# Kernel optimization log

Measured on AMD Instinct MI355X. Metric: run time of the kernel, lower is better.

Reference implementation:

```python
import jax, jax.numpy as jnp
import numpy as np

N_HEADS = 16


def setup_inputs() -> dict:
    key = jax.random.key(0)
    k1, k2, k3 = jax.random.split(key, 3)
    n_embed = 1024
    b, t = 4, 2048
    x = jax.random.normal(k1, (b, t, n_embed), dtype=jnp.float32)
    # Linear weights stored as [in, out]; y = x @ W + b (same math as torch Linear).
    Wqkv = jax.random.normal(k2, (n_embed, 3 * n_embed), dtype=jnp.float32) * (n_embed ** -0.5)
    bqkv = jnp.zeros((3 * n_embed,), dtype=jnp.float32)
    Wout = jax.random.normal(k3, (n_embed, n_embed), dtype=jnp.float32) * (n_embed ** -0.5)
    bout = jnp.zeros((n_embed,), dtype=jnp.float32)
    return {"x": x, "Wqkv": Wqkv, "bqkv": bqkv, "Wout": Wout, "bout": bout}


def reference(x, Wqkv, bqkv, Wout, bout):
    b, t, n_embed = x.shape
    hs = n_embed // N_HEADS
    qkv = x @ Wqkv + bqkv  # [b, t, 3*n_embed]
    q, k, v = jnp.split(qkv, 3, axis=-1)
    # b t (h hs) -> b h t hs
    def to_heads(u):
        return u.reshape(b, t, N_HEADS, hs).transpose(0, 2, 1, 3)
    q, k, v = to_heads(q), to_heads(k), to_heads(v)
    scale = 1.0 / jnp.sqrt(jnp.asarray(hs, dtype=x.dtype))
    scores = jnp.einsum('bhqd,bhkd->bhqk', q, k) * scale  # [b, h, t, t]
    causal = jnp.tril(jnp.ones((t, t), dtype=bool))
    scores = jnp.where(causal, scores, jnp.finfo(scores.dtype).min)
    attn = jax.nn.softmax(scores, axis=-1)
    out = jnp.einsum('bhqk,bhkd->bhqd', attn, v)  # [b, h, t, hs]
    out = out.transpose(0, 2, 1, 3).reshape(b, t, n_embed)  # b h t hs -> b t (h hs)
    return out @ Wout + bout
```

## Files before the change

kernel.cpp:

```cpp
#include <hip/hip_runtime.h>
#include <hip/hip_bf16.h>
#include <stdint.h>

typedef unsigned short u16;
typedef __bf16 bf16x8 __attribute__((ext_vector_type(8)));
typedef float f32x4 __attribute__((ext_vector_type(4)));
typedef u16 ushort8 __attribute__((ext_vector_type(8)));
typedef short short4v __attribute__((ext_vector_type(4)));

__device__ __forceinline__ u16 f2bf(float f) {
    unsigned int u = __builtin_bit_cast(unsigned int, f);
    u += 0x7fffu + ((u >> 16) & 1u);
    return (u16)(u >> 16);
}

#define MFMA16(a, b, c) __builtin_amdgcn_mfma_f32_16x16x32_bf16( \
    __builtin_bit_cast(bf16x8, a), __builtin_bit_cast(bf16x8, b), c, 0, 0, 0)

#if defined(__has_builtin)
#if __has_builtin(__builtin_amdgcn_exp2f)
#define EXP2(x) __builtin_amdgcn_exp2f(x)
#endif
#endif
#ifndef EXP2
#define EXP2(x) __expf((x) * 0.69314718f)
#endif

__device__ __forceinline__ void async16(void* lds, const void* g) {
    __builtin_amdgcn_global_load_lds(
        (const __attribute__((address_space(1))) unsigned int*)(uintptr_t)g,
        (__attribute__((address_space(3))) unsigned int*)(unsigned int)(uintptr_t)lds,
        16, 0, 0);
}

__global__ __launch_bounds__(256) void convert_bf16(
    const float* __restrict__ src, u16* __restrict__ dst)
{
    int i = blockIdx.x * 256 + threadIdx.x;
    float4 f0 = ((const float4*)src)[i * 2];
    float4 f1 = ((const float4*)src)[i * 2 + 1];
    ushort8 v;
    v[0]=f2bf(f0.x); v[1]=f2bf(f0.y); v[2]=f2bf(f0.z); v[3]=f2bf(f0.w);
    v[4]=f2bf(f1.x); v[5]=f2bf(f1.y); v[6]=f2bf(f1.z); v[7]=f2bf(f1.w);
    ((ushort8*)dst)[i] = v;
}

__global__ __launch_bounds__(256) void transpose_convert(
    const float* __restrict__ src, u16* __restrict__ dst, int N, int K)
{
    __shared__ u16 T[64][68];
    const int k0 = blockIdx.x * 64, n0 = blockIdx.y * 64;
    const int tid = threadIdx.x;
    const int rr = tid >> 4, cc = (tid & 15) * 4;
    #pragma unroll
    for (int rnd = 0; rnd < 4; ++rnd) {
        int r = rr + rnd * 16;
        float4 f = *(const float4*)&src[(size_t)(k0 + r) * N + n0 + cc];
        u16 v[4] = {f2bf(f.x), f2bf(f.y), f2bf(f.z), f2bf(f.w)};
        *(unsigned long long*)&T[r][cc] = *(unsigned long long*)v;
    }
    __syncthreads();
    #pragma unroll
    for (int rnd = 0; rnd < 4; ++rnd) {
        int rn = rr + rnd * 16;
        u16 v[4];
        #pragma unroll
        for (int j = 0; j < 4; ++j) v[j] = T[cc + j][rn];
        *(unsigned long long*)&dst[(size_t)(n0 + rn) * K + k0 + cc] =
            *(unsigned long long*)v;
    }
}

__device__ __forceinline__ void gemm_mainloop(
    const u16* __restrict__ A, const u16* __restrict__ Bt,
    u16* As, u16* Bs, int m0, int n0, int tid, f32x4 acc[4][4])
{
    const int lane = tid & 63, w = tid >> 6;
    const int lr = lane & 15, quad = lane >> 4;
    const int wm = w & 1, wn = w >> 1;
    const int grow = lane & 7, gchunk = lane >> 3;

    for (int k0 = 0; k0 < 1024; k0 += 64) {
        __syncthreads();
        #pragma unroll
        for (int r = 0; r < 4; ++r) {
            int rb = w * 4 + r;
            async16(As + rb * 512,
                    A + (size_t)(m0 + rb * 8 + grow) * 1024 + k0 + gchunk * 8);
            async16(Bs + rb * 512,
                    Bt + (size_t)(n0 + rb * 8 + grow) * 1024 + k0 + gchunk * 8);
        }
        __syncthreads();
        #pragma unroll
        for (int kk = 0; kk < 2; ++kk) {
            ushort8 a[4], b[4];
            #pragma unroll
            for (int mt = 0; mt < 4; ++mt) {
                int rb = wm * 8 + mt * 2 + (lr >> 3);
                a[mt] = *(ushort8*)&As[rb * 512 + (kk * 4 + quad) * 64 + (lr & 7) * 8];
            }
            #pragma unroll
            for (int nt = 0; nt < 4; ++nt) {
                int rb = wn * 8 + nt * 2 + (lr >> 3);
                b[nt] = *(ushort8*)&Bs[rb * 512 + (kk * 4 + quad) * 64 + (lr & 7) * 8];
            }
            #pragma unroll
            for (int mt = 0; mt < 4; ++mt)
                #pragma unroll
                for (int nt = 0; nt < 4; ++nt)
                    acc[mt][nt] = MFMA16(a[mt], b[nt], acc[mt][nt]);
        }
    }
}

__global__ __launch_bounds__(256) void qkv_gemm(
    const u16* __restrict__ xb, const u16* __restrict__ Wt,
    const float* __restrict__ bias, u16* __restrict__ qkvb)
{
    __shared__ u16 As[8192], Bs[8192];
    const int m0 = blockIdx.x * 128, n0 = blockIdx.y * 128;
    const int tid = threadIdx.x;
    f32x4 acc[4][4] = {};
    gemm_mainloop(xb, Wt, As, Bs, m0, n0, tid, acc);

    const int lane = tid & 63, w = tid >> 6;
    const int lr = lane & 15, quad = lane >> 4;
    const int wm = w & 1, wn = w >> 1;
    const int which = n0 >> 10;
    float bv[4];
    #pragma unroll
    for (int nt = 0; nt < 4; ++nt) bv[nt] = bias[n0 + wn * 64 + nt * 16 + lr];

    if (which == 2) {
        u16* vT = qkvb + (size_t)2 * 8388608;
        #pragma unroll
        for (int nt = 0; nt < 4; ++nt) {
            int n = n0 + wn * 64 + nt * 16 + lr;
            int hh = (n >> 6) & 15, d = n & 63;
            #pragma unroll
            for (int mt = 0; mt < 4; ++mt) {
                int mbase = m0 + wm * 64 + mt * 16 + quad * 4;
                int b_idx = mbase >> 11, t0 = mbase & 2047;
                short4v o4;
                #pragma unroll
                for (int reg = 0; reg < 4; ++reg)
                    o4[reg] = (short)f2bf(acc[mt][nt][reg] + bv[nt]);
                *(short4v*)&vT[((size_t)(b_idx * 16 + hh) * 64 + d) * 2048 + t0] = o4;
            }
        }
    } else {
        u16* dst = qkvb + (size_t)which * 8388608;
        #pragma unroll
        for (int mt = 0; mt < 4; ++mt)
          #pragma unroll
          for (int nt = 0; nt < 4; ++nt) {
            int n = n0 + wn * 64 + nt * 16 + lr;
            int hh = (n >> 6) & 15, d = n & 63;
            #pragma unroll
            for (int reg = 0; reg < 4; ++reg) {
                int m = m0 + wm * 64 + mt * 16 + quad * 4 + reg;
                int b_idx = m >> 11, t_idx = m & 2047;
                dst[(((size_t)(b_idx * 16 + hh) * 2048 + t_idx) << 6) + d] =
                    f2bf(acc[mt][nt][reg] + bv[nt]);
            }
          }
    }
}

__global__ __launch_bounds__(256) void out_gemm(
    const u16* __restrict__ A, const u16* __restrict__ Wt,
    const float* __restrict__ bias, float* __restrict__ out)
{
    __shared__ u16 As[8192], Bs[8192];
    const int m0 = blockIdx.x * 128, n0 = blockIdx.y * 128;
    const int tid = threadIdx.x;
    f32x4 acc[4][4] = {};
    gemm_mainloop(A, Wt, As, Bs, m0, n0, tid, acc);

    const int lane = tid & 63, w = tid >> 6;
    const int lr = lane & 15, quad = lane >> 4;
    const int wm = w & 1, wn = w >> 1;
    float bv[4];
    #pragma unroll
    for (int nt = 0; nt < 4; ++nt) bv[nt] = bias[n0 + wn * 64 + nt * 16 + lr];
    #pragma unroll
    for (int mt = 0; mt < 4; ++mt)
      #pragma unroll
      for (int nt = 0; nt < 4; ++nt)
        #pragma unroll
        for (int reg = 0; reg < 4; ++reg) {
            int m = m0 + wm * 64 + mt * 16 + quad * 4 + reg;
            int n = n0 + wn * 64 + nt * 16 + lr;
            out[(size_t)m * 1024 + n] = acc[mt][nt][reg] + bv[nt];
        }
}

__global__ __launch_bounds__(256) void attn_kernel(
    const u16* __restrict__ qkvb, u16* __restrict__ o_ws)
{
    const int orig = blockIdx.x + 16 * (blockIdx.y + 16 * blockIdx.z);
    const int work = (orig & 7) * 128 + (orig >> 3);
    const int p = work & 15, h = (work >> 4) & 15, b = work >> 8;
    const size_t bh = (size_t)(b * 16 + h) * 131072;
    const u16* Qb = qkvb + bh;
    const u16* Kb = qkvb + 8388608 + bh;
    const u16* Vt = qkvb + 2 * 8388608 + bh;
    __shared__ u16 Ks[2][4096];
    __shared__ u16 Vts[4096];
    __shared__ u16 Ps[64 * 72];
    const int tid = threadIdx.x, lane = tid & 63, w = tid >> 6;
    const int lr = lane & 15, quad = lane >> 4;
    const int grow = lane & 7, gchunk = lane >> 3;
    const float kscale = 0.125f * 1.44269504f;

    for (int pass = 0; pass < 2; ++pass) {
        const int qt = pass ? (31 - p) : p;
        ushort8 qf[2];
        {
            const u16* qr = Qb + (size_t)(qt * 64 + w * 16 + lr) * 64 + quad * 8;
            qf[0] = *(const ushort8*)qr;
            qf[1] = *(const ushort8*)(qr + 32);
        }
        f32x4 o_acc[4] = {};
        float m_i = -1e30f, l_i = 0.f;
        const int qrow = w * 16 + lr;
        const int bsrc = (lane & 48) + ((lane >> 4) << 2);

        __syncthreads();
        #pragma unroll
        for (int r = 0; r < 2; ++r) {
            int rb = w * 2 + r;
            async16(&Ks[0][rb * 512], Kb + (size_t)(rb * 8 + grow) * 64 + gchunk * 8);
        }

        for (int kt = 0; kt <= qt; ++kt) {
            const int buf = kt & 1;
            __syncthreads();

            #pragma unroll
            for (int r = 0; r < 2; ++r) {
                int rb = w * 2 + r;
                if (kt < qt)
                    async16(&Ks[buf ^ 1][rb * 512],
                            Kb + (size_t)((kt + 1) * 64 + rb * 8 + grow) * 64 + gchunk * 8);
                async16(&Vts[rb * 512],
                        Vt + (size_t)(rb * 8 + grow) * 2048 + kt * 64 + gchunk * 8);
            }

            f32x4 s[4] = {};
            #pragma unroll
            for (int nt = 0; nt < 4; ++nt)
                #pragma unroll
                for (int kk = 0; kk < 2; ++kk) {
                    ushort8 bb = *(ushort8*)&Ks[buf][(nt * 2 + (lr >> 3)) * 512 +
                                                     (kk * 4 + quad) * 64 + (lr & 7) * 8];
                    s[nt] = MFMA16(bb, qf[kk], s[nt]);
                }
            if (kt == qt) {
                #pragma unroll
                for (int nt = 0; nt < 4; ++nt)
                    #pragma unroll
                    for (int reg = 0; reg < 4; ++reg) {
                        int kc = nt * 16 + quad * 4 + reg;
                        s[nt][reg] = (kc > qrow) ? -1e30f : s[nt][reg] * kscale;
                    }
            } else {
                #pragma unroll
                for (int nt = 0; nt < 4; ++nt)
                    #pragma unroll
                    for (int reg = 0; reg < 4; ++reg) s[nt][reg] *= kscale;
            }
            float mx = -1e30f;
            #pragma unroll
            for (int nt = 0; nt < 4; ++nt)
                #pragma unroll
                for (int reg = 0; reg < 4; ++reg) mx = fmaxf(mx, s[nt][reg]);
            mx = fmaxf(mx, __shfl_xor(mx, 16, 64));
            mx = fmaxf(mx, __shfl_xor(mx, 32, 64));
            if (!__all(mx <= m_i + 8.0f)) {
                float mnew = fmaxf(m_i, mx);
                float alpha = EXP2(m_i - mnew);
                m_i = mnew;
                l_i *= alpha;
                #pragma unroll
                for (int reg = 0; reg < 4; ++reg) {
                    float ar = __shfl(alpha, bsrc + reg, 64);
                    #pragma unroll
                    for (int dt = 0; dt < 4; ++dt) o_acc[dt][reg] *= ar;
                }
            }
            float p4[4][4];
            float rs = 0.f;
            #pragma unroll
            for (int nt = 0; nt < 4; ++nt)
                #pragma unroll
                for (int reg = 0; reg < 4; ++reg) {
                    float pv = EXP2(s[nt][reg] - m_i);
                    p4[nt][reg] = pv;
                    rs += pv;
                }
            rs += __shfl_xor(rs, 16, 64);
            rs += __shfl_xor(rs, 32, 64);
            l_i += rs;
            #pragma unroll
            for (int nt = 0; nt < 4; ++nt) {
                u16 v4[4];
                #pragma unroll
                for (int reg = 0; reg < 4; ++reg) v4[reg] = f2bf(p4[nt][reg]);
                *(unsigned long long*)&Ps[qrow * 72 + nt * 16 + quad * 4] =
                    *(unsigned long long*)v4;
            }

            __syncthreads();

            #pragma unroll
            for (int kk = 0; kk < 2; ++kk) {
                ushort8 pa = *(ushort8*)&Ps[(w * 16 + lr) * 72 + kk * 32 + quad * 8];
                #pragma unroll
                for (int dt = 0; dt < 4; ++dt) {
                    ushort8 vb = *(ushort8*)&Vts[(dt * 2 + (lr >> 3)) * 512 +
                                                 (kk * 4 + quad) * 64 + (lr & 7) * 8];
                    o_acc[dt] = MFMA16(pa, vb, o_acc[dt]);
                }
            }
        }

        float rinv = 1.0f / l_i;
        float rl[4];
        #pragma unroll
        for (int reg = 0; reg < 4; ++reg) rl[reg] = __shfl(rinv, bsrc + reg, 64);
        #pragma unroll
        for (int dt = 0; dt < 4; ++dt)
            #pragma unroll
            for (int reg = 0; reg < 4; ++reg) {
                int row = w * 16 + quad * 4 + reg;
                int tq = qt * 64 + row;
                o_ws[((size_t)(b * 2048 + tq) << 10) + h * 64 + dt * 16 + lr] =
                    f2bf(o_acc[dt][reg] * rl[reg]);
            }
    }
}

extern "C" void kernel_launch(void* const* d_in, const int* in_sizes, int n_in,
                              void* d_out, int out_size, void* d_ws, size_t ws_size,
                              hipStream_t stream)
{
    const float* x    = (const float*)d_in[0];
    const float* Wqkv = (const float*)d_in[1];
    const float* bqkv = (const float*)d_in[2];
    const float* Wout = (const float*)d_in[3];
    const float* bout = (const float*)d_in[4];
    float* out = (float*)d_out;

    u16* qkvb = (u16*)d_ws;
    u16* xb   = qkvb + (size_t)3 * 8388608;
    u16* wT   = qkvb + (size_t)4 * 8388608;
    u16* attn_o = xb;

    convert_bf16<<<4096, 256, 0, stream>>>(x, xb);
    transpose_convert<<<dim3(16, 48), 256, 0, stream>>>(Wqkv, wT, 3072, 1024);
    qkv_gemm<<<dim3(64, 24), 256, 0, stream>>>(xb, wT, bqkv, qkvb);
    attn_kernel<<<dim3(16, 16, 4), 256, 0, stream>>>(qkvb, attn_o);
    transpose_convert<<<dim3(16, 16), 256, 0, stream>>>(Wout, wT, 1024, 1024);
    out_gemm<<<dim3(64, 8), 256, 0, stream>>>(attn_o, wT, bout, out);
}
```

Before: 302.8 us.

## Triple-buffer GEMM mainloop with async prefetch and 256x128 tiles

Replaces the synchronous single-buffer GEMM mainloop with a three-stage LDS ring that prefetches two K-tiles ahead and waits using explicit vmcnt counts. Blocks grow to 512 threads computing 256x128 tiles, and s_setprio is raised during the MFMA phase. The aim is to hide global-to-LDS latency and halve redundant B loads per output. In exchange each block uses 144KB of LDS, which together with launch_bounds(512,2) limits occupancy, and the grid has fewer blocks.

Measured after the change: 279.9 us. 1.08x faster.

```diff
diff --git a/kernel.cpp b/kernel.cpp
--- a/kernel.cpp
+++ b/kernel.cpp
@@ -71,38 +71,67 @@
     }
 }
 
-__device__ __forceinline__ void gemm_mainloop(
+#define KT_N 16
+
+__device__ __forceinline__ void stage_tile256(
     const u16* __restrict__ A, const u16* __restrict__ Bt,
-    u16* As, u16* Bs, int m0, int n0, int tid, f32x4 acc[4][4])
+    u16* Lb, int m0, int n0, int k0, int w, int grow, int gchunk)
+{
+    #pragma unroll
+    for (int r = 0; r < 4; ++r) {
+        int rb = w * 4 + r;
+        async16(Lb + rb * 512,
+                A + (size_t)(m0 + rb * 8 + grow) * 1024 + k0 + gchunk * 8);
+    }
+    #pragma unroll
+    for (int r = 0; r < 2; ++r) {
+        int rb = w * 2 + r;
+        async16(Lb + 16384 + rb * 512,
+                Bt + (size_t)(n0 + rb * 8 + grow) * 1024 + k0 + gchunk * 8);
+    }
+}
+
+__device__ __forceinline__ void gemm_mainloop256(
+    const u16* __restrict__ A, const u16* __restrict__ Bt,
+    u16* L, int m0, int n0, int tid, f32x4 acc[4][4])
 {
     const int lane = tid & 63, w = tid >> 6;
     const int lr = lane & 15, quad = lane >> 4;
-    const int wm = w & 1, wn = w >> 1;
+    const int wm = w >> 1, wn = w & 1;
     const int grow = lane & 7, gchunk = lane >> 3;
 
-    for (int k0 = 0; k0 < 1024; k0 += 64) {
-        __syncthreads();
-        #pragma unroll
-        for (int r = 0; r < 4; ++r) {
-            int rb = w * 4 + r;
-            async16(As + rb * 512,
-                    A + (size_t)(m0 + rb * 8 + grow) * 1024 + k0 + gchunk * 8);
-            async16(Bs + rb * 512,
-                    Bt + (size_t)(n0 + rb * 8 + grow) * 1024 + k0 + gchunk * 8);
-        }
-        __syncthreads();
+    stage_tile256(A, Bt, L,         m0, n0, 0,  w, grow, gchunk);
+    stage_tile256(A, Bt, L + 24576, m0, n0, 64, w, grow, gchunk);
+
+    u16* Lc = L;
+    u16* Ls = L + 49152;
+    u16* const Lend = L + 73728;
+
+    for (int t = 0; t < KT_N; ++t) {
+        if (t < KT_N - 2)
+            stage_tile256(A, Bt, Ls, m0, n0, (t + 2) * 64, w, grow, gchunk);
+
+        if (t < KT_N - 2)       asm volatile("s_waitcnt vmcnt(12)" ::: "memory");
+        else if (t == KT_N - 2) asm volatile("s_waitcnt vmcnt(6)"  ::: "memory");
+        else                    asm volatile("s_waitcnt vmcnt(0)"  ::: "memory");
+        __builtin_amdgcn_s_barrier();
+        asm volatile("" ::: "memory");
+
+        const u16* As = Lc;
+        const u16* Bs = Lc + 16384;
+        __builtin_amdgcn_s_setprio(1);
         #pragma unroll
         for (int kk = 0; kk < 2; ++kk) {
             ushort8 a[4], b[4];
             #pragma unroll
             for (int mt = 0; mt < 4; ++mt) {
                 int rb = wm * 8 + mt * 2 + (lr >> 3);
-                a[mt] = *(ushort8*)&As[rb * 512 + (kk * 4 + quad) * 64 + (lr & 7) * 8];
+                a[mt] = *(const ushort8*)&As[rb * 512 + (kk * 4 + quad) * 64 + (lr & 7) * 8];
             }
             #pragma unroll
             for (int nt = 0; nt < 4; ++nt) {
                 int rb = wn * 8 + nt * 2 + (lr >> 3);
-                b[nt] = *(ushort8*)&Bs[rb * 512 + (kk * 4 + quad) * 64 + (lr & 7) * 8];
+                b[nt] = *(const ushort8*)&Bs[rb * 512 + (kk * 4 + quad) * 64 + (lr & 7) * 8];
             }
             #pragma unroll
             for (int mt = 0; mt < 4; ++mt)
@@ -110,22 +139,29 @@
                 for (int nt = 0; nt < 4; ++nt)
                     acc[mt][nt] = MFMA16(a[mt], b[nt], acc[mt][nt]);
         }
-    }
-}
-
-__global__ __launch_bounds__(256) void qkv_gemm(
+        __builtin_amdgcn_s_setprio(0);
+        asm volatile("" ::: "memory");
+        __builtin_amdgcn_s_barrier();
+        asm volatile("" ::: "memory");
+
+        Lc += 24576; if (Lc == Lend) Lc = L;
+        Ls += 24576; if (Ls == Lend) Ls = L;
+    }
+}
+
+__global__ __launch_bounds__(512, 2) void qkv_gemm(
     const u16* __restrict__ xb, const u16* __restrict__ Wt,
     const float* __restrict__ bias, u16* __restrict__ qkvb)
 {
-    __shared__ u16 As[8192], Bs[8192];
-    const int m0 = blockIdx.x * 128, n0 = blockIdx.y * 128;
+    __shared__ u16 L[73728];
+    const int m0 = blockIdx.x * 256, n0 = blockIdx.y * 128;
     const int tid = threadIdx.x;
     f32x4 acc[4][4] = {};
-    gemm_mainloop(xb, Wt, As, Bs, m0, n0, tid, acc);
+    gemm_mainloop256(xb, Wt, L, m0, n0, tid, acc);
 
     const int lane = tid & 63, w = tid >> 6;
     const int lr = lane & 15, quad = lane >> 4;
-    const int wm = w & 1, wn = w >> 1;
+    const int wm = w >> 1, wn = w & 1;
     const int which = n0 >> 10;
     float bv[4];
     #pragma unroll
@@ -167,19 +203,19 @@
     }
 }
 
-__global__ __launch_bounds__(256) void out_gemm(
+__global__ __launch_bounds__(512, 2) void out_gemm(
     const u16* __restrict__ A, const u16* __restrict__ Wt,
     const float* __restrict__ bias, float* __restrict__ out)
 {
-    __shared__ u16 As[8192], Bs[8192];
-    const int m0 = blockIdx.x * 128, n0 = blockIdx.y * 128;
+    __shared__ u16 L[73728];
+    const int m0 = blockIdx.x * 256, n0 = blockIdx.y * 128;
     const int tid = threadIdx.x;
     f32x4 acc[4][4] = {};
-    gemm_mainloop(A, Wt, As, Bs, m0, n0, tid, acc);
+    gemm_mainloop256(A, Wt, L, m0, n0, tid, acc);
 
     const int lane = tid & 63, w = tid >> 6;
     const int lr = lane & 15, quad = lane >> 4;
-    const int wm = w & 1, wn = w >> 1;
+    const int wm = w >> 1, wn = w & 1;
     float bv[4];
     #pragma unroll
     for (int nt = 0; nt < 4; ++nt) bv[nt] = bias[n0 + wn * 64 + nt * 16 + lr];
@@ -359,8 +395,8 @@
 
     convert_bf16<<<4096, 256, 0, stream>>>(x, xb);
     transpose_convert<<<dim3(16, 48), 256, 0, stream>>>(Wqkv, wT, 3072, 1024);
-    qkv_gemm<<<dim3(64, 24), 256, 0, stream>>>(xb, wT, bqkv, qkvb);
+    qkv_gemm<<<dim3(32, 24), 512, 0, stream>>>(xb, wT, bqkv, qkvb);
     attn_kernel<<<dim3(16, 16, 4), 256, 0, stream>>>(qkvb, attn_o);
     transpose_convert<<<dim3(16, 16), 256, 0, stream>>>(Wout, wT, 1024, 1024);
-    out_gemm<<<dim3(64, 8), 256, 0, stream>>>(attn_o, wT, bout, out);
-}
+    out_gemm<<<dim3(32, 8), 512, 0, stream>>>(attn_o, wT, bout, out);
+}
```

## Rewrite GEMMs as 256x256 double-buffered 8-wave pipelined mainloop

Applied to the files above, without the earlier changes.

Both projection GEMMs move from 128x128 tiles with 4 waves and single-buffered LDS to 256x256 tiles with 8 waves, 128KB of double-buffered LDS, and a phased schedule. The next K tile is prefetched asynchronously while MFMAs run, with explicit barriers, waitcnt and setprio around each MFMA cluster. This is meant to hide global load latency and increase data reuse per tile. The trade-off is fewer blocks: out_gemm launches only 128 blocks, which may underfill the GPU, and the larger accumulator raises register pressure.

Result: no change. 303.9 us (+0.4%).

```diff
diff --git a/kernel.cpp b/kernel.cpp
--- a/kernel.cpp
+++ b/kernel.cpp
@@ -71,61 +71,136 @@
     }
 }
 
-__device__ __forceinline__ void gemm_mainloop(
+#define QK_TILES 16
+
+__device__ __forceinline__ void stage256(
     const u16* __restrict__ A, const u16* __restrict__ Bt,
-    u16* As, u16* Bs, int m0, int n0, int tid, f32x4 acc[4][4])
+    u16* Lb, int m0, int n0, int k0, int w, int grow, int gchunk)
+{
+    #pragma unroll
+    for (int r = 0; r < 4; ++r) {
+        int rb = w * 4 + r;
+        async16(Lb + rb * 512,
+                A + (size_t)(m0 + rb * 8 + grow) * 1024 + k0 + gchunk * 8);
+    }
+    #pragma unroll
+    for (int r = 0; r < 4; ++r) {
+        int rb = w * 4 + r;
+        async16(Lb + 16384 + rb * 512,
+                Bt + (size_t)(n0 + rb * 8 + grow) * 1024 + k0 + gchunk * 8);
+    }
+}
+
+__device__ __forceinline__ void gemm_mainloop_8ph(
+    const u16* __restrict__ A, const u16* __restrict__ Bt,
+    u16* L, int m0, int n0, int tid, f32x4 acc[8][4])
 {
     const int lane = tid & 63, w = tid >> 6;
     const int lr = lane & 15, quad = lane >> 4;
-    const int wm = w & 1, wn = w >> 1;
+    const int wm = w >> 2, wn = w & 3;
     const int grow = lane & 7, gchunk = lane >> 3;
-
-    for (int k0 = 0; k0 < 1024; k0 += 64) {
-        __syncthreads();
-        #pragma unroll
-        for (int r = 0; r < 4; ++r) {
-            int rb = w * 4 + r;
-            async16(As + rb * 512,
-                    A + (size_t)(m0 + rb * 8 + grow) * 1024 + k0 + gchunk * 8);
-            async16(Bs + rb * 512,
-                    Bt + (size_t)(n0 + rb * 8 + grow) * 1024 + k0 + gchunk * 8);
-        }
-        __syncthreads();
-        #pragma unroll
-        for (int kk = 0; kk < 2; ++kk) {
-            ushort8 a[4], b[4];
-            #pragma unroll
-            for (int mt = 0; mt < 4; ++mt) {
-                int rb = wm * 8 + mt * 2 + (lr >> 3);
-                a[mt] = *(ushort8*)&As[rb * 512 + (kk * 4 + quad) * 64 + (lr & 7) * 8];
-            }
-            #pragma unroll
-            for (int nt = 0; nt < 4; ++nt) {
-                int rb = wn * 8 + nt * 2 + (lr >> 3);
-                b[nt] = *(ushort8*)&Bs[rb * 512 + (kk * 4 + quad) * 64 + (lr & 7) * 8];
-            }
-            #pragma unroll
-            for (int mt = 0; mt < 4; ++mt)
-                #pragma unroll
-                for (int nt = 0; nt < 4; ++nt)
-                    acc[mt][nt] = MFMA16(a[mt], b[nt], acc[mt][nt]);
-        }
-    }
-}
-
-__global__ __launch_bounds__(256) void qkv_gemm(
+    const int arb = wm * 16 + (lr >> 3);
+    const int brb = wn * 8 + (lr >> 3);
+    const int foff = (lr & 7) * 8;
+
+    stage256(A, Bt, L, m0, n0, 0, w, grow, gchunk);
+    asm volatile("s_waitcnt vmcnt(0)" ::: "memory");
+    __builtin_amdgcn_s_barrier();
+    asm volatile("" ::: "memory");
+
+    #pragma unroll 2
+    for (int t = 0; t < QK_TILES; ++t) {
+        const u16* As = L + (t & 1) * 32768;
+        const u16* Bs = As + 16384;
+        ushort8 a[8], b[4];
+
+        if (t + 1 < QK_TILES)
+            stage256(A, Bt, L + ((t + 1) & 1) * 32768, m0, n0, (t + 1) * 64,
+                     w, grow, gchunk);
+        #pragma unroll
+        for (int nt = 0; nt < 4; ++nt)
+            b[nt] = *(const ushort8*)&Bs[(brb + nt * 2) * 512 + quad * 64 + foff];
+        #pragma unroll
+        for (int mt = 0; mt < 4; ++mt)
+            a[mt] = *(const ushort8*)&As[(arb + mt * 2) * 512 + quad * 64 + foff];
+        __builtin_amdgcn_s_barrier();
+        asm volatile("s_waitcnt lgkmcnt(0)" ::: "memory");
+        __builtin_amdgcn_sched_barrier(0);
+        __builtin_amdgcn_s_setprio(1);
+        #pragma unroll
+        for (int mt = 0; mt < 4; ++mt)
+            #pragma unroll
+            for (int nt = 0; nt < 4; ++nt)
+                acc[mt][nt] = MFMA16(a[mt], b[nt], acc[mt][nt]);
+        __builtin_amdgcn_s_setprio(0);
+        __builtin_amdgcn_s_barrier();
+
+        #pragma unroll
+        for (int mt = 4; mt < 8; ++mt)
+            a[mt] = *(const ushort8*)&As[(arb + mt * 2) * 512 + quad * 64 + foff];
+        __builtin_amdgcn_s_barrier();
+        asm volatile("s_waitcnt lgkmcnt(0)" ::: "memory");
+        __builtin_amdgcn_sched_barrier(0);
+        __builtin_amdgcn_s_setprio(1);
+        #pragma unroll
+        for (int mt = 4; mt < 8; ++mt)
+            #pragma unroll
+            for (int nt = 0; nt < 4; ++nt)
+                acc[mt][nt] = MFMA16(a[mt], b[nt], acc[mt][nt]);
+        __builtin_amdgcn_s_setprio(0);
+        __builtin_amdgcn_s_barrier();
+
+        #pragma unroll
+        for (int nt = 0; nt < 4; ++nt)
+            b[nt] = *(const ushort8*)&Bs[(brb + nt * 2) * 512 + 256 + quad * 64 + foff];
+        #pragma unroll
+        for (int mt = 0; mt < 4; ++mt)
+            a[mt] = *(const ushort8*)&As[(arb + mt * 2) * 512 + 256 + quad * 64 + foff];
+        __builtin_amdgcn_s_barrier();
+        asm volatile("s_waitcnt lgkmcnt(0)" ::: "memory");
+        __builtin_amdgcn_sched_barrier(0);
+        __builtin_amdgcn_s_setprio(1);
+        #pragma unroll
+        for (int mt = 0; mt < 4; ++mt)
+            #pragma unroll
+            for (int nt = 0; nt < 4; ++nt)
+                acc[mt][nt] = MFMA16(a[mt], b[nt], acc[mt][nt]);
+        __builtin_amdgcn_s_setprio(0);
+        __builtin_amdgcn_s_barrier();
+
+        #pragma unroll
+        for (int mt = 4; mt < 8; ++mt)
+            a[mt] = *(const ushort8*)&As[(arb + mt * 2) * 512 + 256 + quad * 64 + foff];
+        if (t + 1 < QK_TILES)
+            asm volatile("s_waitcnt vmcnt(0)" ::: "memory");
+        __builtin_amdgcn_s_barrier();
+        asm volatile("s_waitcnt lgkmcnt(0)" ::: "memory");
+        __builtin_amdgcn_sched_barrier(0);
+        __builtin_amdgcn_s_setprio(1);
+        #pragma unroll
+        for (int mt = 4; mt < 8; ++mt)
+            #pragma unroll
+            for (int nt = 0; nt < 4; ++nt)
+                acc[mt][nt] = MFMA16(a[mt], b[nt], acc[mt][nt]);
+        __builtin_amdgcn_s_setprio(0);
+        __builtin_amdgcn_s_barrier();
+        asm volatile("" ::: "memory");
+    }
+}
+
+__global__ __launch_bounds__(512, 2) void qkv_gemm(
     const u16* __restrict__ xb, const u16* __restrict__ Wt,
     const float* __restrict__ bias, u16* __restrict__ qkvb)
 {
-    __shared__ u16 As[8192], Bs[8192];
-    const int m0 = blockIdx.x * 128, n0 = blockIdx.y * 128;
+    __shared__ u16 L[65536];
+    const int m0 = blockIdx.x * 256, n0 = blockIdx.y * 256;
     const int tid = threadIdx.x;
-    f32x4 acc[4][4] = {};
-    gemm_mainloop(xb, Wt, As, Bs, m0, n0, tid, acc);
+    f32x4 acc[8][4] = {};
+    gemm_mainloop_8ph(xb, Wt, L, m0, n0, tid, acc);
 
     const int lane = tid & 63, w = tid >> 6;
     const int lr = lane & 15, quad = lane >> 4;
-    const int wm = w & 1, wn = w >> 1;
+    const int wm = w >> 2, wn = w & 3;
     const int which = n0 >> 10;
     float bv[4];
     #pragma unroll
@@ -138,8 +213,8 @@
             int n = n0 + wn * 64 + nt * 16 + lr;
             int hh = (n >> 6) & 15, d = n & 63;
             #pragma unroll
-            for (int mt = 0; mt < 4; ++mt) {
-                int mbase = m0 + wm * 64 + mt * 16 + quad * 4;
+            for (int mt = 0; mt < 8; ++mt) {
+                int mbase = m0 + wm * 128 + mt * 16 + quad * 4;
                 int b_idx = mbase >> 11, t0 = mbase & 2047;
                 short4v o4;
                 #pragma unroll
@@ -151,14 +226,14 @@
     } else {
         u16* dst = qkvb + (size_t)which * 8388608;
         #pragma unroll
-        for (int mt = 0; mt < 4; ++mt)
+        for (int mt = 0; mt < 8; ++mt)
           #pragma unroll
           for (int nt = 0; nt < 4; ++nt) {
             int n = n0 + wn * 64 + nt * 16 + lr;
             int hh = (n >> 6) & 15, d = n & 63;
             #pragma unroll
             for (int reg = 0; reg < 4; ++reg) {
-                int m = m0 + wm * 64 + mt * 16 + quad * 4 + reg;
+                int m = m0 + wm * 128 + mt * 16 + quad * 4 + reg;
                 int b_idx = m >> 11, t_idx = m & 2047;
                 dst[(((size_t)(b_idx * 16 + hh) * 2048 + t_idx) << 6) + d] =
                     f2bf(acc[mt][nt][reg] + bv[nt]);
@@ -167,29 +242,29 @@
     }
 }
 
-__global__ __launch_bounds__(256) void out_gemm(
+__global__ __launch_bounds__(512, 2) void out_gemm(
     const u16* __restrict__ A, const u16* __restrict__ Wt,
     const float* __restrict__ bias, float* __restrict__ out)
 {
-    __shared__ u16 As[8192], Bs[8192];
-    const int m0 = blockIdx.x * 128, n0 = blockIdx.y * 128;
+    __shared__ u16 L[65536];
+    const int m0 = blockIdx.x * 256, n0 = blockIdx.y * 256;
     const int tid = threadIdx.x;
-    f32x4 acc[4][4] = {};
-    gemm_mainloop(A, Wt, As, Bs, m0, n0, tid, acc);
+    f32x4 acc[8][4] = {};
+    gemm_mainloop_8ph(A, Wt, L, m0, n0, tid, acc);
 
     const int lane = tid & 63, w = tid >> 6;
     const int lr = lane & 15, quad = lane >> 4;
-    const int wm = w & 1, wn = w >> 1;
+    const int wm = w >> 2, wn = w & 3;
     float bv[4];
     #pragma unroll
     for (int nt = 0; nt < 4; ++nt) bv[nt] = bias[n0 + wn * 64 + nt * 16 + lr];
     #pragma unroll
-    for (int mt = 0; mt < 4; ++mt)
+    for (int mt = 0; mt < 8; ++mt)
       #pragma unroll
       for (int nt = 0; nt < 4; ++nt)
         #pragma unroll
         for (int reg = 0; reg < 4; ++reg) {
-            int m = m0 + wm * 64 + mt * 16 + quad * 4 + reg;
+            int m = m0 + wm * 128 + mt * 16 + quad * 4 + reg;
             int n = n0 + wn * 64 + nt * 16 + lr;
             out[(size_t)m * 1024 + n] = acc[mt][nt][reg] + bv[nt];
         }
@@ -359,8 +434,8 @@
 
     convert_bf16<<<4096, 256, 0, stream>>>(x, xb);
     transpose_convert<<<dim3(16, 48), 256, 0, stream>>>(Wqkv, wT, 3072, 1024);
-    qkv_gemm<<<dim3(64, 24), 256, 0, stream>>>(xb, wT, bqkv, qkvb);
+    qkv_gemm<<<dim3(32, 12), 512, 0, stream>>>(xb, wT, bqkv, qkvb);
     attn_kernel<<<dim3(16, 16, 4), 256, 0, stream>>>(qkvb, attn_o);
     transpose_convert<<<dim3(16, 16), 256, 0, stream>>>(Wout, wT, 1024, 1024);
-    out_gemm<<<dim3(64, 8), 256, 0, stream>>>(attn_o, wT, bout, out);
-}
+    out_gemm<<<dim3(32, 4), 512, 0, stream>>>(attn_o, wT, bout, out);
+}
```
